# Optimization experiments

Measured on AMD Instinct MI355X. Metric: run time of the kernel, lower is better.

Reference implementation:

```python
import jax, jax.numpy as jnp
import numpy as np

N_NODES = 100000
N_EDGES = 3200000
D_FEAT = 512
HIDDEN = 16
N_CLASSES = 16


def setup_inputs() -> dict:
    key = jax.random.key(0)
    ks = jax.random.split(key, 6)
    x = jax.random.normal(ks[0], (N_NODES, D_FEAT), dtype=jnp.float32)
    edge_index = jax.random.randint(ks[1], (2, N_EDGES), 0, N_NODES, dtype=jnp.int64)
    edge_weight = jax.random.uniform(ks[2], (N_EDGES,), dtype=jnp.float32)
    W1 = jax.random.normal(ks[3], (D_FEAT, HIDDEN), dtype=jnp.float32) * (1.0 / np.sqrt(D_FEAT))
    b1 = jnp.zeros((HIDDEN,), dtype=jnp.float32)
    W2 = jax.random.normal(ks[4], (HIDDEN, N_CLASSES), dtype=jnp.float32) * (1.0 / np.sqrt(HIDDEN))
    b2 = jnp.zeros((N_CLASSES,), dtype=jnp.float32)
    return {"x": x, "edge_index": edge_index, "edge_weight": edge_weight,
            "W1": W1, "b1": b1, "W2": W2, "b2": b2}


def _gcn_conv(h, src, dst, edge_weight, W, b, num_nodes):
    # linear transform then edge-weighted scatter-add: out[dst] += w_e * (h W)[src]
    h = h @ W                                   # [N, out]
    msg = edge_weight[:, None] * h[src]         # [E, out] gather + scale
    out = jax.ops.segment_sum(msg, dst, num_segments=num_nodes)  # scatter-add
    return out + b


def reference(x, edge_index, edge_weight, W1, b1, W2, b2):
    src, dst = edge_index[0], edge_index[1]
    n = x.shape[0]
    h = jax.nn.relu(_gcn_conv(x, src, dst, edge_weight, W1, b1, n))
    # dropout is identity in eval mode
    h = _gcn_conv(h, src, dst, edge_weight, W2, b2, n)
    return jax.nn.log_softmax(h, axis=1)
```

## Files before the change

### kernel.cpp

```cpp
#include <hip/hip_runtime.h>
#include <math.h>

#define NN 100000
#define DF 512
#define HID 16
#define NBUCK 392
#define EPB 4096
#define BCAP 7800

#define TN 256
#define KC 64
#define NCH (DF / KC)
#define LROW 65

__device__ int g_idx64;

__global__ void detect_idx_kernel(const long long* __restrict__ idx) {
    int lane = threadIdx.x;
    int ok = 1;
    for (int i = lane; i < 128; i += 64) {
        long long v = idx[i];
        if (v < 0 || v >= NN) ok = 0;
    }
    unsigned long long m = __ballot(ok);
    if (lane == 0) g_idx64 = (m == ~0ULL);
}

__global__ __launch_bounds__(512) void gemm1_kernel(
    const float* __restrict__ x, const float* __restrict__ W1,
    float* __restrict__ h1, int nN)
{
    __shared__ float sx[TN * LROW];
    const int t = threadIdx.x;
    const int hf = __builtin_amdgcn_readfirstlane(t >> 8);
    const int node = t & (TN - 1);
    const int node0 = blockIdx.x * TN;
    const int tr = t >> 4;
    const int tq = t & 15;

    const float4* x4 = (const float4*)x;
    int rowg[8];
#pragma unroll
    for (int i = 0; i < 8; ++i) {
        int r = node0 + i * 32 + tr;
        rowg[i] = (r < nN) ? r : (nN - 1);
    }

    float acc[16];
#pragma unroll
    for (int c = 0; c < 16; ++c) acc[c] = 0.f;

    float4 pfA[8], pfB[8];

    auto issue = [&](float4* buf, int kc) {
#pragma unroll
        for (int i = 0; i < 8; ++i)
            buf[i] = x4[(size_t)rowg[i] * (DF / 4) + kc * 16 + tq];
    };
    auto step = [&](float4* buf, int kc) {
#pragma unroll
        for (int i = 0; i < 8; ++i) {
            int a = (i * 32 + tr) * LROW + tq * 4;
            sx[a + 0] = buf[i].x; sx[a + 1] = buf[i].y;
            sx[a + 2] = buf[i].z; sx[a + 3] = buf[i].w;
        }
        __syncthreads();
        if (kc + 2 < NCH) issue(buf, kc + 2);
        const float* wb = W1 + (kc * KC + hf * 32) * HID;
        const float* xr = sx + node * LROW + hf * 32;
#pragma unroll 4
        for (int kk = 0; kk < 32; ++kk) {
            float s = xr[kk];
            const float* wr = wb + kk * HID;
#pragma unroll
            for (int c = 0; c < 16; ++c)
                acc[c] = fmaf(s, wr[c], acc[c]);
        }
        __syncthreads();
    };

    issue(pfA, 0);
    issue(pfB, 1);
#pragma unroll
    for (int kc2 = 0; kc2 < NCH; kc2 += 2) {
        step(pfA, kc2);
        step(pfB, kc2 + 1);
    }

    float* part = sx;
    if (hf == 1) {
#pragma unroll
        for (int c = 0; c < 16; ++c) part[node * 17 + c] = acc[c];
    }
    __syncthreads();
    if (hf == 0) {
        int gn = node0 + node;
        if (gn < nN) {
#pragma unroll
            for (int c = 0; c < 16; ++c) acc[c] += part[node * 17 + c];
            float4* o = (float4*)(h1 + (size_t)gn * HID);
#pragma unroll
            for (int g = 0; g < 4; ++g)
                o[g] = make_float4(acc[g * 4 + 0], acc[g * 4 + 1],
                                   acc[g * 4 + 2], acc[g * 4 + 3]);
        }
    }
}

__global__ __launch_bounds__(256) void bucket_hist_kernel(
    const void* __restrict__ eidx, int* __restrict__ bcnt, int nE)
{
    __shared__ int h[NBUCK];
    for (int i = threadIdx.x; i < NBUCK; i += 256) h[i] = 0;
    __syncthreads();
    const int i64 = g_idx64;
    int stride = gridDim.x * 256;
    int tid = blockIdx.x * 256 + threadIdx.x;
    if ((nE & 1) == 0) {
        int nE2 = nE >> 1;
        if (i64) {
            const int4* dp = (const int4*)((const long long*)eidx + nE);
            for (int i = tid; i < nE2; i += stride) {
                int4 d = dp[i];
                if (d.y == 0 && (unsigned)d.x < (unsigned)NN) atomicAdd(&h[d.x >> 8], 1);
                if (d.w == 0 && (unsigned)d.z < (unsigned)NN) atomicAdd(&h[d.z >> 8], 1);
            }
        } else {
            const int2* dp = (const int2*)((const int*)eidx + nE);
            for (int i = tid; i < nE2; i += stride) {
                int2 d = dp[i];
                if ((unsigned)d.x < (unsigned)NN) atomicAdd(&h[d.x >> 8], 1);
                if ((unsigned)d.y < (unsigned)NN) atomicAdd(&h[d.y >> 8], 1);
            }
        }
    } else {
        for (int e = tid; e < nE; e += stride) {
            int d;
            if (i64) d = (int)((const long long*)eidx)[nE + e];
            else     d = ((const int*)eidx)[nE + e];
            if ((unsigned)d < (unsigned)NN) atomicAdd(&h[d >> 8], 1);
        }
    }
    __syncthreads();
    for (int i = threadIdx.x; i < NBUCK; i += 256)
        if (h[i]) atomicAdd(&bcnt[i], h[i]);
}

__global__ __launch_bounds__(512) void bucket_scan_kernel(
    const int* __restrict__ bcnt, int* __restrict__ bbase,
    int* __restrict__ cursor, int* __restrict__ rowStart)
{
    __shared__ int s[512];
    int t = threadIdx.x;
    int v = (t < NBUCK) ? bcnt[t] : 0;
    s[t] = v;
    __syncthreads();
    for (int off = 1; off < 512; off <<= 1) {
        int u = (t >= off) ? s[t - off] : 0;
        __syncthreads();
        s[t] += u;
        __syncthreads();
    }
    int excl = s[t] - v;
    if (t < NBUCK) { bbase[t] = excl; cursor[t] = excl; }
    if (t == NBUCK) bbase[t] = excl;
    if (t == NBUCK) rowStart[NN] = excl;
}

__global__ __launch_bounds__(256) void bucketA_kernel(
    const void* __restrict__ eidx, const float* __restrict__ ew,
    int* __restrict__ cursor, int2* __restrict__ packed, int nE)
{
    __shared__ int cnt[NBUCK];
    __shared__ int base[NBUCK];
    int t = threadIdx.x;
    for (int i = t; i < NBUCK; i += 256) cnt[i] = 0;
    __syncthreads();

    const int e0 = blockIdx.x * EPB;
    const int i64 = g_idx64;
    int lo[16]; float wv[16]; int bk[16];
#pragma unroll
    for (int i = 0; i < 16; ++i) {
        int e = e0 + t + i * 256;
        bk[i] = -1;
        if (e < nE) {
            int s, d;
            if (i64) {
                const long long* p = (const long long*)eidx;
                s = (int)p[e]; d = (int)p[nE + e];
            } else {
                const int* p = (const int*)eidx;
                s = p[e]; d = p[nE + e];
            }
            if ((unsigned)d < (unsigned)NN) {
                float w = ew[e];
                if ((unsigned)s >= (unsigned)NN) { s = 0; w = 0.f; }
                bk[i] = d >> 8;
                lo[i] = s | ((d & 255) << 20);
                wv[i] = w;
                atomicAdd(&cnt[bk[i]], 1);
            }
        }
    }
    __syncthreads();
    for (int i = t; i < NBUCK; i += 256)
        base[i] = (cnt[i] > 0) ? atomicAdd(&cursor[i], cnt[i]) : 0;
    __syncthreads();
    for (int i = t; i < NBUCK; i += 256) cnt[i] = 0;
    __syncthreads();
#pragma unroll
    for (int i = 0; i < 16; ++i) {
        if (bk[i] >= 0) {
            int r = atomicAdd(&cnt[bk[i]], 1);
            packed[base[bk[i]] + r] = make_int2(lo[i], __float_as_int(wv[i]));
        }
    }
}

__global__ __launch_bounds__(256) void bucketB_kernel(
    const int2* __restrict__ packed, const int* __restrict__ bbase,
    int* __restrict__ rowStart, int2* __restrict__ se, int nN)
{
    __shared__ int hcnt[256];
    __shared__ int wtot[4];
    __shared__ int2 stage[BCAP];
    int b = blockIdx.x;
    int t = threadIdx.x;
    int beg = bbase[b], end = bbase[b + 1];
    int cnt = end - beg;

    hcnt[t] = 0;
    __syncthreads();
    for (int i = t; i < cnt; i += 256) {
        int2 e = packed[beg + i];
        if (i < BCAP) stage[i] = e;
        atomicAdd(&hcnt[(e.x >> 20) & 255], 1);
    }
    __syncthreads();

    int v = hcnt[t];
    int incl = v;
#pragma unroll
    for (int off = 1; off < 64; off <<= 1) {
        int u = __shfl_up(incl, off, 64);
        if ((t & 63) >= off) incl += u;
    }
    if ((t & 63) == 63) wtot[t >> 6] = incl;
    __syncthreads();
    int woff = 0;
#pragma unroll
    for (int w = 0; w < 4; ++w) if (w < (t >> 6)) woff += wtot[w];
    int excl = incl - v + woff;

    int node = b * 256 + t;
    if (node < nN) rowStart[node] = beg + excl;
    __syncthreads();
    hcnt[t] = beg + excl;
    __syncthreads();

    for (int i = t; i < cnt; i += 256) {
        int2 e = (i < BCAP) ? stage[i] : packed[beg + i];
        int dl = (e.x >> 20) & 255;
        int pos = atomicAdd(&hcnt[dl], 1);
        se[pos] = make_int2(e.x & 0xFFFFF, e.y);
    }
}

template <int EPI>
__global__ __launch_bounds__(256) void gather_fused_kernel(
    const int* __restrict__ rowStart, const int2* __restrict__ se,
    const float* __restrict__ h, const float* __restrict__ bias,
    const float* __restrict__ Wn, float* __restrict__ outp, int nN)
{
    __shared__ float sW[256];
    __shared__ float sb[16];
    if (EPI == 0) sW[threadIdx.x] = Wn[threadIdx.x];
    if (threadIdx.x < 16) sb[threadIdx.x] = bias[threadIdx.x];
    __syncthreads();

    int t = blockIdx.x * 256 + threadIdx.x;
    int n = t >> 2;
    if (n >= nN) return;
    int c4 = t & 3;
    int beg = rowStart[n], end = rowStart[n + 1];
    const float4* h4 = (const float4*)h;

    float ax = 0.f, ay = 0.f, az = 0.f, aw = 0.f;
    int p = beg;
    for (; p + 8 <= end; p += 8) {
        int2 ee[8];
        float4 vv[8];
#pragma unroll
        for (int j = 0; j < 8; ++j) ee[j] = se[p + j];
#pragma unroll
        for (int j = 0; j < 8; ++j)
            vv[j] = h4[(size_t)(unsigned)ee[j].x * 4 + c4];
#pragma unroll
        for (int j = 0; j < 8; ++j) {
            float w = __int_as_float(ee[j].y);
            ax = fmaf(w, vv[j].x, ax); ay = fmaf(w, vv[j].y, ay);
            az = fmaf(w, vv[j].z, az); aw = fmaf(w, vv[j].w, aw);
        }
    }
    if (p + 4 <= end) {
        int2 ee[4];
        float4 vv[4];
#pragma unroll
        for (int j = 0; j < 4; ++j) ee[j] = se[p + j];
#pragma unroll
        for (int j = 0; j < 4; ++j)
            vv[j] = h4[(size_t)(unsigned)ee[j].x * 4 + c4];
#pragma unroll
        for (int j = 0; j < 4; ++j) {
            float w = __int_as_float(ee[j].y);
            ax = fmaf(w, vv[j].x, ax); ay = fmaf(w, vv[j].y, ay);
            az = fmaf(w, vv[j].z, az); aw = fmaf(w, vv[j].w, aw);
        }
        p += 4;
    }
    for (; p < end; ++p) {
        int2 e = se[p];
        float4 v = h4[(size_t)(unsigned)e.x * 4 + c4];
        float w = __int_as_float(e.y);
        ax = fmaf(w, v.x, ax); ay = fmaf(w, v.y, ay);
        az = fmaf(w, v.z, az); aw = fmaf(w, v.w, aw);
    }

    int lane = threadIdx.x & 63;
    int lb = lane & ~3;

    if (EPI == 0) {
        float v0 = fmaxf(ax + sb[c4 * 4 + 0], 0.f);
        float v1 = fmaxf(ay + sb[c4 * 4 + 1], 0.f);
        float v2 = fmaxf(az + sb[c4 * 4 + 2], 0.f);
        float v3 = fmaxf(aw + sb[c4 * 4 + 3], 0.f);
        float vk[16];
#pragma unroll
        for (int j = 0; j < 4; ++j) {
            vk[4 * j + 0] = __shfl(v0, lb + j, 64);
            vk[4 * j + 1] = __shfl(v1, lb + j, 64);
            vk[4 * j + 2] = __shfl(v2, lb + j, 64);
            vk[4 * j + 3] = __shfl(v3, lb + j, 64);
        }
        float o0 = 0.f, o1 = 0.f, o2 = 0.f, o3 = 0.f;
#pragma unroll
        for (int k = 0; k < 16; ++k) {
            float s = vk[k];
            o0 = fmaf(s, sW[k * 16 + c4 * 4 + 0], o0);
            o1 = fmaf(s, sW[k * 16 + c4 * 4 + 1], o1);
            o2 = fmaf(s, sW[k * 16 + c4 * 4 + 2], o2);
            o3 = fmaf(s, sW[k * 16 + c4 * 4 + 3], o3);
        }
        ((float4*)outp)[(size_t)n * 4 + c4] = make_float4(o0, o1, o2, o3);
    } else {
        float v0 = ax + sb[c4 * 4 + 0];
        float v1 = ay + sb[c4 * 4 + 1];
        float v2 = az + sb[c4 * 4 + 2];
        float v3 = aw + sb[c4 * 4 + 3];
        float m = fmaxf(fmaxf(v0, v1), fmaxf(v2, v3));
        m = fmaxf(m, __shfl_xor(m, 1, 64));
        m = fmaxf(m, __shfl_xor(m, 2, 64));
        float s = expf(v0 - m) + expf(v1 - m) + expf(v2 - m) + expf(v3 - m);
        s += __shfl_xor(s, 1, 64);
        s += __shfl_xor(s, 2, 64);
        float l = m + logf(s);
        ((float4*)outp)[(size_t)n * 4 + c4] =
            make_float4(v0 - l, v1 - l, v2 - l, v3 - l);
    }
}

extern "C" void kernel_launch(void* const* d_in, const int* in_sizes, int n_in,
                              void* d_out, int out_size, void* d_ws, size_t ws_size,
                              hipStream_t stream)
{
    const float* x  = (const float*)d_in[0];
    const void*  ei = d_in[1];
    const float* ew = (const float*)d_in[2];
    const float* W1 = (const float*)d_in[3];
    const float* b1 = (const float*)d_in[4];
    const float* W2 = (const float*)d_in[5];
    const float* b2 = (const float*)d_in[6];
    float* out = (float*)d_out;

    const int N = NN;
    const int E = in_sizes[2];

    const size_t featB = (size_t)N * HID * sizeof(float);
    const size_t rowB  = (((size_t)(N + 1) * 4) + 255) & ~255ULL;
    const size_t bkB   = (((size_t)(NBUCK + 1) * 4) + 255) & ~255ULL;
    const size_t seB   = ((size_t)E * 8 + 255) & ~255ULL;

    char* w = (char*)d_ws;
    float* buf0 = (float*)w;      w += (featB + 255) & ~255ULL;
    float* buf1 = (float*)w;      w += (featB + 255) & ~255ULL;
    int*   rowStart = (int*)w;    w += rowB;
    int*   bcnt = (int*)w;        w += bkB;
    int*   bbase = (int*)w;       w += bkB;
    int*   cursor = (int*)w;      w += bkB;
    int2*  se = (int2*)w;         w += seB;
    int2*  packed = (int2*)w;     w += seB;

    detect_idx_kernel<<<1, 64, 0, stream>>>((const long long*)ei);
    gemm1_kernel<<<(N + TN - 1) / TN, 512, 0, stream>>>(x, W1, buf0, N);

    const int nblocks4 = (N * 4 + 255) / 256;

    hipMemsetAsync(bcnt, 0, (size_t)NBUCK * 4, stream);
    bucket_hist_kernel<<<256, 256, 0, stream>>>(ei, bcnt, E);
    bucket_scan_kernel<<<1, 512, 0, stream>>>(bcnt, bbase, cursor, rowStart);
    bucketA_kernel<<<(E + EPB - 1) / EPB, 256, 0, stream>>>(ei, ew, cursor, packed, E);
    bucketB_kernel<<<NBUCK, 256, 0, stream>>>(packed, bbase, rowStart, se, N);

    gather_fused_kernel<0><<<nblocks4, 256, 0, stream>>>(rowStart, se, buf0, b1, W2, buf1, N);
    gather_fused_kernel<1><<<nblocks4, 256, 0, stream>>>(rowStart, se, buf1, b2, W2, out, N);
}
```

Before: 502.8 us.

## Fuse GEMM1 with bucket histogram, per-wave GEMM tiles, vectorize edge loads

Merges the layer-1 GEMM and the destination-bucket histogram into one launch, with extra blocks doing the histogram. The histogram counter reset moves into the index-detect kernel in place of a memset. The GEMM is restructured so each wave owns 64 nodes with its own shared-memory slice, dropping the block-wide barriers and the two-half reduction. The bucketing pass also loads edge pairs with wider vector loads. This cuts launch overhead and lets the histogram overlap the GEMM, at the cost of higher register pressure from the fully unrolled inner loop.

```diff
diff --git a/kernel.cpp b/kernel.cpp
--- a/kernel.cpp
+++ b/kernel.cpp
@@ -8,14 +8,16 @@
 #define EPB 4096
 #define BCAP 7800
 
-#define TN 256
-#define KC 64
-#define NCH (DF / KC)
-#define LROW 65
+#define GTN 256
+#define GKC 32
+#define GNCH (DF / GKC)
+#define GLROW 33
+#define HISTB 128
 
 __device__ int g_idx64;
 
-__global__ void detect_idx_kernel(const long long* __restrict__ idx) {
+__global__ void detect_idx_kernel(const long long* __restrict__ idx,
+                                  int* __restrict__ bcnt) {
     int lane = threadIdx.x;
     int ok = 1;
     for (int i = lane; i < 128; i += 64) {
@@ -24,25 +26,66 @@
     }
     unsigned long long m = __ballot(ok);
     if (lane == 0) g_idx64 = (m == ~0ULL);
-}
-
-__global__ __launch_bounds__(512) void gemm1_kernel(
+    for (int i = lane; i < NBUCK; i += 64) bcnt[i] = 0;
+}
+
+__global__ __launch_bounds__(256, 4) void front_kernel(
     const float* __restrict__ x, const float* __restrict__ W1,
-    float* __restrict__ h1, int nN)
-{
-    __shared__ float sx[TN * LROW];
+    float* __restrict__ h1, const void* __restrict__ eidx,
+    int* __restrict__ bcnt, int nN, int nE, int gemmBlocks)
+{
+    __shared__ float sx[4][64 * GLROW];
+    __shared__ int hh[NBUCK];
+    const int b = blockIdx.x;
     const int t = threadIdx.x;
-    const int hf = __builtin_amdgcn_readfirstlane(t >> 8);
-    const int node = t & (TN - 1);
-    const int node0 = blockIdx.x * TN;
-    const int tr = t >> 4;
-    const int tq = t & 15;
+
+    if (b >= gemmBlocks) {
+        for (int i = t; i < NBUCK; i += 256) hh[i] = 0;
+        __syncthreads();
+        const int i64 = g_idx64;
+        int stride = HISTB * 256;
+        int tid = (b - gemmBlocks) * 256 + t;
+        if ((nE & 1) == 0) {
+            int nE2 = nE >> 1;
+            if (i64) {
+                const int4* dp = (const int4*)((const long long*)eidx + nE);
+                for (int i = tid; i < nE2; i += stride) {
+                    int4 d = dp[i];
+                    if (d.y == 0 && (unsigned)d.x < (unsigned)NN) atomicAdd(&hh[d.x >> 8], 1);
+                    if (d.w == 0 && (unsigned)d.z < (unsigned)NN) atomicAdd(&hh[d.z >> 8], 1);
+                }
+            } else {
+                const int2* dp = (const int2*)((const int*)eidx + nE);
+                for (int i = tid; i < nE2; i += stride) {
+                    int2 d = dp[i];
+                    if ((unsigned)d.x < (unsigned)NN) atomicAdd(&hh[d.x >> 8], 1);
+                    if ((unsigned)d.y < (unsigned)NN) atomicAdd(&hh[d.y >> 8], 1);
+                }
+            }
+        } else {
+            for (int e = tid; e < nE; e += stride) {
+                int d;
+                if (i64) d = (int)((const long long*)eidx)[nE + e];
+                else     d = ((const int*)eidx)[nE + e];
+                if ((unsigned)d < (unsigned)NN) atomicAdd(&hh[d >> 8], 1);
+            }
+        }
+        __syncthreads();
+        for (int i = t; i < NBUCK; i += 256)
+            if (hh[i]) atomicAdd(&bcnt[i], hh[i]);
+        return;
+    }
+
+    const int w = t >> 6;
+    const int l = t & 63;
+    float* sw = sx[w];
+    const int wbase = b * GTN + w * 64;
 
     const float4* x4 = (const float4*)x;
     int rowg[8];
 #pragma unroll
     for (int i = 0; i < 8; ++i) {
-        int r = node0 + i * 32 + tr;
+        int r = wbase + i * 8 + (l >> 3);
         rowg[i] = (r < nN) ? r : (nN - 1);
     }
 
@@ -55,95 +98,48 @@
     auto issue = [&](float4* buf, int kc) {
 #pragma unroll
         for (int i = 0; i < 8; ++i)
-            buf[i] = x4[(size_t)rowg[i] * (DF / 4) + kc * 16 + tq];
+            buf[i] = x4[(size_t)rowg[i] * (DF / 4) + kc * 8 + (l & 7)];
     };
-    auto step = [&](float4* buf, int kc) {
+    auto stage = [&](float4* buf) {
 #pragma unroll
         for (int i = 0; i < 8; ++i) {
-            int a = (i * 32 + tr) * LROW + tq * 4;
-            sx[a + 0] = buf[i].x; sx[a + 1] = buf[i].y;
-            sx[a + 2] = buf[i].z; sx[a + 3] = buf[i].w;
-        }
-        __syncthreads();
-        if (kc + 2 < NCH) issue(buf, kc + 2);
-        const float* wb = W1 + (kc * KC + hf * 32) * HID;
-        const float* xr = sx + node * LROW + hf * 32;
-#pragma unroll 4
-        for (int kk = 0; kk < 32; ++kk) {
+            int a = (i * 8 + (l >> 3)) * GLROW + (l & 7) * 4;
+            sw[a + 0] = buf[i].x; sw[a + 1] = buf[i].y;
+            sw[a + 2] = buf[i].z; sw[a + 3] = buf[i].w;
+        }
+    };
+    auto compute = [&](int kc) {
+        const float* xr = sw + l * GLROW;
+        const float* wb = W1 + kc * GKC * HID;
+#pragma unroll
+        for (int kk = 0; kk < GKC; ++kk) {
             float s = xr[kk];
             const float* wr = wb + kk * HID;
 #pragma unroll
             for (int c = 0; c < 16; ++c)
                 acc[c] = fmaf(s, wr[c], acc[c]);
         }
-        __syncthreads();
     };
 
     issue(pfA, 0);
     issue(pfB, 1);
-#pragma unroll
-    for (int kc2 = 0; kc2 < NCH; kc2 += 2) {
-        step(pfA, kc2);
-        step(pfB, kc2 + 1);
-    }
-
-    float* part = sx;
-    if (hf == 1) {
-#pragma unroll
-        for (int c = 0; c < 16; ++c) part[node * 17 + c] = acc[c];
-    }
-    __syncthreads();
-    if (hf == 0) {
-        int gn = node0 + node;
-        if (gn < nN) {
-#pragma unroll
-            for (int c = 0; c < 16; ++c) acc[c] += part[node * 17 + c];
-            float4* o = (float4*)(h1 + (size_t)gn * HID);
-#pragma unroll
-            for (int g = 0; g < 4; ++g)
-                o[g] = make_float4(acc[g * 4 + 0], acc[g * 4 + 1],
-                                   acc[g * 4 + 2], acc[g * 4 + 3]);
-        }
-    }
-}
-
-__global__ __launch_bounds__(256) void bucket_hist_kernel(
-    const void* __restrict__ eidx, int* __restrict__ bcnt, int nE)
-{
-    __shared__ int h[NBUCK];
-    for (int i = threadIdx.x; i < NBUCK; i += 256) h[i] = 0;
-    __syncthreads();
-    const int i64 = g_idx64;
-    int stride = gridDim.x * 256;
-    int tid = blockIdx.x * 256 + threadIdx.x;
-    if ((nE & 1) == 0) {
-        int nE2 = nE >> 1;
-        if (i64) {
-            const int4* dp = (const int4*)((const long long*)eidx + nE);
-            for (int i = tid; i < nE2; i += stride) {
-                int4 d = dp[i];
-                if (d.y == 0 && (unsigned)d.x < (unsigned)NN) atomicAdd(&h[d.x >> 8], 1);
-                if (d.w == 0 && (unsigned)d.z < (unsigned)NN) atomicAdd(&h[d.z >> 8], 1);
-            }
-        } else {
-            const int2* dp = (const int2*)((const int*)eidx + nE);
-            for (int i = tid; i < nE2; i += stride) {
-                int2 d = dp[i];
-                if ((unsigned)d.x < (unsigned)NN) atomicAdd(&h[d.x >> 8], 1);
-                if ((unsigned)d.y < (unsigned)NN) atomicAdd(&h[d.y >> 8], 1);
-            }
-        }
-    } else {
-        for (int e = tid; e < nE; e += stride) {
-            int d;
-            if (i64) d = (int)((const long long*)eidx)[nE + e];
-            else     d = ((const int*)eidx)[nE + e];
-            if ((unsigned)d < (unsigned)NN) atomicAdd(&h[d >> 8], 1);
-        }
-    }
-    __syncthreads();
-    for (int i = threadIdx.x; i < NBUCK; i += 256)
-        if (h[i]) atomicAdd(&bcnt[i], h[i]);
+    for (int kc = 0; kc < GNCH; kc += 2) {
+        stage(pfA);
+        if (kc + 2 < GNCH) issue(pfA, kc + 2);
+        compute(kc);
+        stage(pfB);
+        if (kc + 3 < GNCH) issue(pfB, kc + 3);
+        compute(kc + 1);
+    }
+
+    int gn = wbase + l;
+    if (gn < nN) {
+        float4* o = (float4*)(h1 + (size_t)gn * HID);
+#pragma unroll
+        for (int g = 0; g < 4; ++g)
+            o[g] = make_float4(acc[g * 4 + 0], acc[g * 4 + 1],
+                               acc[g * 4 + 2], acc[g * 4 + 3]);
+    }
 }
 
 __global__ __launch_bounds__(512) void bucket_scan_kernel(
@@ -180,26 +176,62 @@
     const int e0 = blockIdx.x * EPB;
     const int i64 = g_idx64;
     int lo[16]; float wv[16]; int bk[16];
-#pragma unroll
-    for (int i = 0; i < 16; ++i) {
-        int e = e0 + t + i * 256;
-        bk[i] = -1;
-        if (e < nE) {
-            int s, d;
+
+    auto classify = [&](int slot, int s, int d, float w, bool valid) {
+        bk[slot] = -1;
+        if (valid && (unsigned)d < (unsigned)NN) {
+            if ((unsigned)s >= (unsigned)NN) { s = 0; w = 0.f; }
+            bk[slot] = d >> 8;
+            lo[slot] = s | ((d & 255) << 20);
+            wv[slot] = w;
+            atomicAdd(&cnt[bk[slot]], 1);
+        }
+    };
+
+    if ((nE & 1) == 0) {
+        const int p0 = e0 >> 1;
+        const int nP = nE >> 1;
+        const float2* wp = (const float2*)ew;
+#pragma unroll
+        for (int i = 0; i < 8; ++i) {
+            int p = p0 + t + i * 256;
+            bool v = p < nP;
+            int pc = v ? p : 0;
+            int s0, s1, d0, d1;
+            bool ok0 = v, ok1 = v;
             if (i64) {
-                const long long* p = (const long long*)eidx;
-                s = (int)p[e]; d = (int)p[nE + e];
+                const int4* sp = (const int4*)eidx;
+                const int4* dp = (const int4*)((const long long*)eidx + nE);
+                int4 s4 = sp[pc]; int4 d4 = dp[pc];
+                s0 = s4.x; s1 = s4.z; d0 = d4.x; d1 = d4.z;
+                ok0 = ok0 && (d4.y == 0); ok1 = ok1 && (d4.w == 0);
+                if (s4.y != 0) s0 = -1;
+                if (s4.w != 0) s1 = -1;
             } else {
-                const int* p = (const int*)eidx;
-                s = p[e]; d = p[nE + e];
+                const int2* sp = (const int2*)eidx;
+                const int2* dp = (const int2*)((const int*)eidx + nE);
+                int2 s2 = sp[pc]; int2 d2 = dp[pc];
+                s0 = s2.x; s1 = s2.y; d0 = d2.x; d1 = d2.y;
             }
-            if ((unsigned)d < (unsigned)NN) {
-                float w = ew[e];
-                if ((unsigned)s >= (unsigned)NN) { s = 0; w = 0.f; }
-                bk[i] = d >> 8;
-                lo[i] = s | ((d & 255) << 20);
-                wv[i] = w;
-                atomicAdd(&cnt[bk[i]], 1);
+            float2 w2 = wp[pc];
+            classify(2 * i + 0, s0, d0, w2.x, ok0);
+            classify(2 * i + 1, s1, d1, w2.y, ok1);
+        }
+    } else {
+#pragma unroll
+        for (int i = 0; i < 16; ++i) {
+            int e = e0 + t + i * 256;
+            bk[i] = -1;
+            if (e < nE) {
+                int s, d;
+                if (i64) {
+                    const long long* p = (const long long*)eidx;
+                    s = (int)p[e]; d = (int)p[nE + e];
+                } else {
+                    const int* p = (const int*)eidx;
+                    s = p[e]; d = p[nE + e];
+                }
+                classify(i, s, d, ew[e], true);
             }
         }
     }
@@ -401,17 +433,17 @@
     int2*  se = (int2*)w;         w += seB;
     int2*  packed = (int2*)w;     w += seB;
 
-    detect_idx_kernel<<<1, 64, 0, stream>>>((const long long*)ei);
-    gemm1_kernel<<<(N + TN - 1) / TN, 512, 0, stream>>>(x, W1, buf0, N);
-
-    const int nblocks4 = (N * 4 + 255) / 256;
-
-    hipMemsetAsync(bcnt, 0, (size_t)NBUCK * 4, stream);
-    bucket_hist_kernel<<<256, 256, 0, stream>>>(ei, bcnt, E);
+    detect_idx_kernel<<<1, 64, 0, stream>>>((const long long*)ei, bcnt);
+
+    const int gemmBlocks = (N + GTN - 1) / GTN;
+    front_kernel<<<gemmBlocks + HISTB, 256, 0, stream>>>(
+        x, W1, buf0, ei, bcnt, N, E, gemmBlocks);
+
     bucket_scan_kernel<<<1, 512, 0, stream>>>(bcnt, bbase, cursor, rowStart);
     bucketA_kernel<<<(E + EPB - 1) / EPB, 256, 0, stream>>>(ei, ew, cursor, packed, E);
     bucketB_kernel<<<NBUCK, 256, 0, stream>>>(packed, bbase, rowStart, se, N);
 
+    const int nblocks4 = (N * 4 + 255) / 256;
     gather_fused_kernel<0><<<nblocks4, 256, 0, stream>>>(rowStart, se, buf0, b1, W2, buf1, N);
     gather_fused_kernel<1><<<nblocks4, 256, 0, stream>>>(rowStart, se, buf1, b2, W2, out, N);
 }
```

Measured after the change: 569.1 us. +13.2%, slower.
